# Optimization experiments

Measured on AMD Instinct MI355X. Metric: run time of the kernel, lower is better.

The kernel has to match this reference:

```python
import jax, jax.numpy as jnp
import numpy as np

# Canonical DAG: L topological levels of N nodes each; every node in level l>0
# has K predecessors in level l-1, each edge carrying a scalar weight.
# Input nodes (level 0) take x columns directly (no activation), matching the
# torch module. Output = activations of the (sorted) last-level nodes.

B, N, K, L = 1024, 5000, 16, 10  # batch, nodes/level, fan-in, levels
NEG_SLOPE = 0.1                  # LeakyReLU(0.1) as in the module


def setup_inputs() -> dict:
    key = jax.random.key(0)
    k_x, k_s, k_w, k_b = jax.random.split(key, 4)
    x = jax.random.normal(k_x, (B, N), dtype=jnp.float32)
    # predecessor indices into the previous level, per level 1..L-1
    src_idx = jax.random.randint(k_s, (L - 1, N, K), 0, N)
    # scalar edge weights and node biases ~ N(0, 0.1), as in __init__
    weights = jax.random.normal(k_w, (L - 1, N, K), dtype=jnp.float32) * 0.1
    biases = jax.random.normal(k_b, (L - 1, N), dtype=jnp.float32) * 0.1
    return {"x": x, "src_idx": src_idx, "weights": weights, "biases": biases}


def reference(x, src_idx, weights, biases):
    b, n = x.shape
    k = src_idx.shape[-1]

    def level(act, params):
        s, w, bias = params  # s,w: [N,K], bias: [N]
        # gather predecessor activations: [B, N, K]
        gathered = jnp.take(act, s.reshape(-1), axis=1).reshape(b, n, k)
        # weighted sum over predecessors + bias, then LeakyReLU(0.1)
        pre = jnp.einsum('bnk,nk->bn', gathered, w) + bias
        return jax.nn.leaky_relu(pre, NEG_SLOPE), None

    out, _ = jax.lax.scan(level, x, (src_idx, weights, biases))
    return out  # [B, N] activations of output nodes (sorted order)
```

## Files before the change

### kernel.cpp

```cpp
#include <hip/hip_runtime.h>


#define TB 1024
#define TN 5000
#define TK 16
#define TLV 9
#define CPG 4
#define NG  (TB / CPG)
#define LT  1024
#define NPANEL ((TN + 63) / 64)
#define PEL (NPANEL * TK * 64)

typedef unsigned int u32;
typedef unsigned short u16;
typedef _Float16 h2 __attribute__((ext_vector_type(2)));

__device__ __forceinline__ h2 u2h(u32 v) { return __builtin_bit_cast(h2, v); }
__device__ __forceinline__ u32 h2u(h2 h) { return __builtin_bit_cast(u32, h); }
__device__ __forceinline__ u32 packf(float a, float b) {
    h2 h; h.x = (_Float16)a; h.y = (_Float16)b;
    return h2u(h);
}

__global__ __launch_bounds__(256) void k_pack(
    const int* __restrict__ idx, const float* __restrict__ w,
    u32* __restrict__ pe)
{
    const int wid  = (blockIdx.x * 256 + threadIdx.x) >> 6;
    const int lane = threadIdx.x & 63;
    const int l = wid / NPANEL;
    const int p = wid % NPANEL;
    if (l >= TLV) return;
    const int n = p * 64 + lane;

    u32 ev[TK];
    if (n < TN) {
        const size_t base = ((size_t)l * TN + n) * TK;
        #pragma unroll
        for (int k = 0; k < TK; ++k) {
            const u32 s = (u32)idx[base + k];
            h2 hw; hw.x = (_Float16)w[base + k]; hw.y = (_Float16)0.0f;
            ev[k] = (s * 8u) | (h2u(hw) << 16);
        }
    } else {
        #pragma unroll
        for (int k = 0; k < TK; ++k) ev[k] = 0;
    }

    #pragma unroll
    for (int round = 0; round < TK; ++round) {
        const int start = round & 1;
        #pragma unroll
        for (int i = start; i + 1 < TK; i += 2) {
            const u32 a = ev[i], b = ev[i + 1];
            const bool swp = ((b >> 3) & 15u) < ((a >> 3) & 15u);
            ev[i]     = swp ? b : a;
            ev[i + 1] = swp ? a : b;
        }
    }

    u32* dst = pe + (size_t)l * PEL + (size_t)p * (TK * 64) + lane;
    const int rot = lane & 15;
    #pragma unroll
    for (int r = 0; r < TK; ++r)
        dst[((r - rot) & 15) * 64] = ev[r];
}

__global__ __launch_bounds__(LT) void k_fused(
    const float* __restrict__ x,
    float* __restrict__ out,
    const u32* __restrict__ pe,
    const float* __restrict__ biases)
{
    __shared__ uint2 buf[2][TN];
    const int g = blockIdx.x;
    const int t = threadIdx.x;

    {
        const float* xp0 = x + (size_t)(g * CPG + 0) * TN;
        const float* xp1 = x + (size_t)(g * CPG + 1) * TN;
        const float* xp2 = x + (size_t)(g * CPG + 2) * TN;
        const float* xp3 = x + (size_t)(g * CPG + 3) * TN;
        for (int n = t; n < TN; n += LT) {
            uint2 v;
            v.x = packf(xp0[n], xp1[n]);
            v.y = packf(xp2[n], xp3[n]);
            buf[0][n] = v;
        }
    }
    __syncthreads();

    int cur = 0;
    for (int l = 0; l < TLV; ++l) {
        const u32*   ep_l = pe + (size_t)l * PEL;
        const float* b_l  = biases + (size_t)l * TN;
        const char*  base = reinterpret_cast<const char*>(buf[cur]);
        for (int n = t; n < TN; n += LT) {
            const u32* ep = ep_l + (n >> 6) * (TK * 64) + (n & 63);
            const float bvf = b_l[n];
            h2 bb; bb.x = (_Float16)bvf; bb.y = (_Float16)bvf;
            h2 a01 = bb, a23 = bb;

            #pragma unroll
            for (int k = 0; k < TK; ++k) {
                const u32 e  = ep[k * 64];
                const u32 s8 = e & 0xffffu;
                const h2 w2 = u2h(__builtin_amdgcn_perm(e, e, 0x03020302u));
                const uint2 av = *reinterpret_cast<const uint2*>(base + s8);
                a01 = w2 * u2h(av.x) + a01;
                a23 = w2 * u2h(av.y) + a23;
            }

            h2 tenth; tenth.x = (_Float16)0.1f; tenth.y = (_Float16)0.1f;
            a01 = __builtin_elementwise_max(a01, a01 * tenth);
            a23 = __builtin_elementwise_max(a23, a23 * tenth);

            uint2 r; r.x = h2u(a01); r.y = h2u(a23);
            buf[cur ^ 1][n] = r;
        }
        __syncthreads();
        cur ^= 1;
    }

    {
        float* op0 = out + (size_t)(g * CPG + 0) * TN;
        float* op1 = out + (size_t)(g * CPG + 1) * TN;
        float* op2 = out + (size_t)(g * CPG + 2) * TN;
        float* op3 = out + (size_t)(g * CPG + 3) * TN;
        for (int n = t; n < TN; n += LT) {
            const uint2 v = buf[cur][n];
            h2 h;
            h = u2h(v.x); op0[n] = (float)h.x; op1[n] = (float)h.y;
            h = u2h(v.y); op2[n] = (float)h.x; op3[n] = (float)h.y;
        }
    }
}

extern "C" void kernel_launch(void* const* d_in, const int* in_sizes, int n_in,
                              void* d_out, int out_size, void* d_ws, size_t ws_size,
                              hipStream_t stream)
{
    const float* x       = (const float*)d_in[0];
    const int*   src_idx = (const int*)  d_in[1];
    const float* weights = (const float*)d_in[2];
    const float* biases  = (const float*)d_in[3];
    float* out = (float*)d_out;

    u32* pe = (u32*)d_ws;

    {
        const int nwaves  = TLV * NPANEL;
        const int nblocks = (nwaves + 3) / 4;
        hipLaunchKernelGGL(k_pack, dim3(nblocks), dim3(256), 0, stream,
                           src_idx, weights, pe);
    }
    hipLaunchKernelGGL(k_fused, dim3(NG), dim3(LT), 0, stream,
                       x, out, pe, biases);
}
```

Measured before the change: 128.6 us.

## Duplicate LDS activations and pick a copy per edge to cut bank conflicts

Each level's activations are now stored twice in shared memory, and the pack kernel assigns each edge to one of the two copies. The choice uses a wave ballot and rank over the low source-index bits, so lanes that would hit the same bank pair are split between the copies; this replaces the previous per-lane sort and rotation. Edge records are now stored contiguously per node, so the fused kernel reads them as four 16-byte vector loads instead of strided scalar loads. The cost is twice as many LDS writes per level and doubling the shared buffer to about 156 KB, which sits close to the per-CU LDS limit.

```diff
diff --git a/kernel.cpp b/kernel.cpp
--- a/kernel.cpp
+++ b/kernel.cpp
@@ -13,6 +13,7 @@
 
 typedef unsigned int u32;
 typedef unsigned short u16;
+typedef unsigned long long u64;
 typedef _Float16 h2 __attribute__((ext_vector_type(2)));
 
 __device__ __forceinline__ h2 u2h(u32 v) { return __builtin_bit_cast(h2, v); }
@@ -32,38 +33,41 @@
     const int p = wid % NPANEL;
     if (l >= TLV) return;
     const int n = p * 64 + lane;
+    const bool valid = (n < TN);
 
-    u32 ev[TK];
-    if (n < TN) {
-        const size_t base = ((size_t)l * TN + n) * TK;
+    u32 sv[TK];
+    u32 hw[TK];
+    {
+        const size_t base = ((size_t)l * TN + (valid ? n : 0)) * TK;
         #pragma unroll
         for (int k = 0; k < TK; ++k) {
-            const u32 s = (u32)idx[base + k];
-            h2 hw; hw.x = (_Float16)w[base + k]; hw.y = (_Float16)0.0f;
-            ev[k] = (s * 8u) | (h2u(hw) << 16);
-        }
-    } else {
-        #pragma unroll
-        for (int k = 0; k < TK; ++k) ev[k] = 0;
-    }
-
-    #pragma unroll
-    for (int round = 0; round < TK; ++round) {
-        const int start = round & 1;
-        #pragma unroll
-        for (int i = start; i + 1 < TK; i += 2) {
-            const u32 a = ev[i], b = ev[i + 1];
-            const bool swp = ((b >> 3) & 15u) < ((a >> 3) & 15u);
-            ev[i]     = swp ? b : a;
-            ev[i + 1] = swp ? a : b;
+            sv[k] = valid ? (u32)idx[base + k] : 0u;
+            h2 h; h.x = (_Float16)(valid ? w[base + k] : 0.0f); h.y = (_Float16)0.0f;
+            hw[k] = h2u(h);
         }
     }
 
-    u32* dst = pe + (size_t)l * PEL + (size_t)p * (TK * 64) + lane;
-    const int rot = lane & 15;
+    const u64 lt_mask = (lane == 0) ? 0ull : (~0ull >> (64 - lane));
+    u32 ev[TK];
     #pragma unroll
-    for (int r = 0; r < TK; ++r)
-        dst[((r - rot) & 15) * 64] = ev[r];
+    for (int k = 0; k < TK; ++k) {
+        const u32 c  = sv[k] & 15u;
+        const u32 pr = c & 7u;
+        const u32 hi = c >> 3;
+        int rank = 0;
+        #pragma unroll
+        for (u32 q = 0; q < 8; ++q) {
+            const u64 m = __ballot(pr == q);
+            if (pr == q) rank = __popcll(m & lt_mask);
+        }
+        const u32 tgt = (u32)(rank & 1);
+        const u32 b   = (tgt != hi) ? 1u : 0u;
+        ev[k] = (sv[k] + b * (u32)TN) | (hw[k] << 16);
+    }
+
+    u32* dst = pe + (size_t)l * PEL + (size_t)p * (TK * 64) + lane * TK;
+    #pragma unroll
+    for (int k = 0; k < TK; ++k) dst[k] = ev[k];
 }
 
 __global__ __launch_bounds__(LT) void k_fused(
@@ -72,7 +76,7 @@
     const u32* __restrict__ pe,
     const float* __restrict__ biases)
 {
-    __shared__ uint2 buf[2][TN];
+    __shared__ uint2 buf[2][2 * TN];
     const int g = blockIdx.x;
     const int t = threadIdx.x;
 
@@ -85,7 +89,8 @@
             uint2 v;
             v.x = packf(xp0[n], xp1[n]);
             v.y = packf(xp2[n], xp3[n]);
-            buf[0][n] = v;
+            buf[0][n]      = v;
+            buf[0][TN + n] = v;
         }
     }
     __syncthreads();
@@ -96,17 +101,27 @@
         const float* b_l  = biases + (size_t)l * TN;
         const char*  base = reinterpret_cast<const char*>(buf[cur]);
         for (int n = t; n < TN; n += LT) {
-            const u32* ep = ep_l + (n >> 6) * (TK * 64) + (n & 63);
+            const uint4* ep = reinterpret_cast<const uint4*>(
+                ep_l + (size_t)(n >> 6) * (TK * 64) + (n & 63) * TK);
+            const uint4 e0 = ep[0];
+            const uint4 e1 = ep[1];
+            const uint4 e2 = ep[2];
+            const uint4 e3 = ep[3];
+            const u32 es[TK] = {e0.x, e0.y, e0.z, e0.w,
+                                e1.x, e1.y, e1.z, e1.w,
+                                e2.x, e2.y, e2.z, e2.w,
+                                e3.x, e3.y, e3.z, e3.w};
+
             const float bvf = b_l[n];
             h2 bb; bb.x = (_Float16)bvf; bb.y = (_Float16)bvf;
             h2 a01 = bb, a23 = bb;
 
             #pragma unroll
             for (int k = 0; k < TK; ++k) {
-                const u32 e  = ep[k * 64];
-                const u32 s8 = e & 0xffffu;
+                const u32 e  = es[k];
+                const u32 off = (e & 0x3fffu) << 3;
                 const h2 w2 = u2h(__builtin_amdgcn_perm(e, e, 0x03020302u));
-                const uint2 av = *reinterpret_cast<const uint2*>(base + s8);
+                const uint2 av = *reinterpret_cast<const uint2*>(base + off);
                 a01 = w2 * u2h(av.x) + a01;
                 a23 = w2 * u2h(av.y) + a23;
             }
@@ -116,7 +131,8 @@
             a23 = __builtin_elementwise_max(a23, a23 * tenth);
 
             uint2 r; r.x = h2u(a01); r.y = h2u(a23);
-            buf[cur ^ 1][n] = r;
+            buf[cur ^ 1][n]      = r;
+            buf[cur ^ 1][TN + n] = r;
         }
         __syncthreads();
         cur ^= 1;
```

After: 135.2 us. +5.1%, slower.
